# Kernel tuning notes

Measured on AMD Instinct MI355X. Metric: run time of the kernel, lower is better.

Reference implementation:

```python
import jax, jax.numpy as jnp
import numpy as np


def _binarize_ste(w):
    # forward: sign(w) in {-1, +1}; backward: identity (straight-through)
    wb = jnp.where(w >= 0, 1.0, -1.0).astype(w.dtype)
    return w + jax.lax.stop_gradient(wb - w)


def setup_inputs() -> dict:
    key = jax.random.key(0)
    k1, k2 = jax.random.split(key)
    IN, OUT, N = 2048, 2048, 8192
    x = jax.random.normal(k1, (N, IN), dtype=jnp.float32)
    # kaiming_uniform-like init: U(-bound, bound), bound = sqrt(6/in)*? (gain sqrt(5) default in torch)
    bound = float(np.sqrt(6.0 / IN))
    weight = jax.random.uniform(k2, (OUT, IN), dtype=jnp.float32, minval=-bound, maxval=bound)
    bias = jnp.zeros((OUT,), dtype=jnp.float32)
    return {"x": x, "weight": weight, "bias": bias}


def reference(x, weight, bias):
    w_binary = _binarize_ste(weight)  # [out, in], values in {-1, +1}
    # F.linear: x @ W^T + b
    return jnp.einsum('ni,oi->no', x, w_binary) + bias
```

## Files before the change

kernel.cpp:

```cpp
#include <hip/hip_runtime.h>
#include <stdint.h>


typedef __bf16 bf16x8 __attribute__((ext_vector_type(8)));
typedef float f32x4 __attribute__((ext_vector_type(4)));

typedef const __attribute__((address_space(1))) void* gas_ptr;
typedef __attribute__((address_space(3))) void* lds_ptr;

__device__ __forceinline__ unsigned short f2bf_rne(float f) {
    unsigned int u = __builtin_bit_cast(unsigned int, f);
    u += 0x7fffu + ((u >> 16) & 1u);
    return (unsigned short)(u >> 16);
}

__global__ __launch_bounds__(256) void cvt_x_kernel(const float* __restrict__ in,
                                                    unsigned short* __restrict__ out,
                                                    int n8) {
    int i = blockIdx.x * 256 + threadIdx.x;
    if (i >= n8) return;
    const float4* p = reinterpret_cast<const float4*>(in + (size_t)i * 8);
    float4 f0 = p[0], f1 = p[1];
    union { unsigned short s[8]; uint4 v; } o;
    o.s[0] = f2bf_rne(f0.x); o.s[1] = f2bf_rne(f0.y);
    o.s[2] = f2bf_rne(f0.z); o.s[3] = f2bf_rne(f0.w);
    o.s[4] = f2bf_rne(f1.x); o.s[5] = f2bf_rne(f1.y);
    o.s[6] = f2bf_rne(f1.z); o.s[7] = f2bf_rne(f1.w);
    *reinterpret_cast<uint4*>(out + (size_t)i * 8) = o.v;
}

__global__ __launch_bounds__(256) void bin_w_kernel(const float* __restrict__ in,
                                                    unsigned short* __restrict__ out,
                                                    int n4) {
    int i = blockIdx.x * 256 + threadIdx.x;
    if (i >= n4) return;
    float4 f = reinterpret_cast<const float4*>(in)[i];
    union { unsigned short s[4]; uint2 v; } o;
    o.s[0] = (f.x >= 0.f) ? 0x3F80u : 0xBF80u;
    o.s[1] = (f.y >= 0.f) ? 0x3F80u : 0xBF80u;
    o.s[2] = (f.z >= 0.f) ? 0x3F80u : 0xBF80u;
    o.s[3] = (f.w >= 0.f) ? 0x3F80u : 0xBF80u;
    reinterpret_cast<uint2*>(out)[i] = o.v;
}

#define WAITVM(N) asm volatile("s_waitcnt vmcnt(" #N ")" ::: "memory")

__device__ __forceinline__ void block_bar() {
    asm volatile("" ::: "memory");
    __builtin_amdgcn_s_barrier();
    asm volatile("" ::: "memory");
}

__global__ __launch_bounds__(512, 2) void gemm_bin_kernel(
    const unsigned short* __restrict__ A,
    const unsigned short* __restrict__ B,
    const float* __restrict__ bias,
    float* __restrict__ C,
    int M, int N, int K)
{
    __shared__ __align__(16) unsigned char smem_raw[131072];
    unsigned short* const sm = (unsigned short*)smem_raw;

    const int tid  = threadIdx.x;
    const int lane = tid & 63;
    const int wave = tid >> 6;
    const int wm   = wave >> 2;
    const int wn   = wave & 3;
    const int bm   = blockIdx.y;
    const int bn   = blockIdx.x;

    const unsigned short* __restrict__ Agb = A + (size_t)(bm * 256) * K;
    const unsigned short* __restrict__ Bgb = B + (size_t)(bn * 256) * K;

    const int r15 = lane & 15;
    const int kc  = lane >> 4;
    const int sw  = ((r15 >> 2) & 1) << 1;

    const int baseA0 = wm * 8192 + r15 * 64 + ((kc    ) ^ sw) * 8;
    const int baseA1 = wm * 8192 + r15 * 64 + ((kc + 4) ^ sw) * 8;
    const int bBq    = 16384 + (wn >> 1) * 8192 + (wn & 1) * 4096 + r15 * 64;
    const int baseB0 = bBq + ((kc    ) ^ sw) * 8;
    const int baseB1 = bBq + ((kc + 4) ^ sw) * 8;

    int gsoff[2], ldoff[2];
#pragma unroll
    for (int j = 0; j < 2; ++j) {
        const int g  = j * 512 + tid;
        const int rl = g >> 3;
        const int c  = (g & 7) ^ (((rl >> 2) & 1) << 1);
        gsoff[j] = rl * K + c * 8;
        ldoff[j] = g * 8;
    }

    const int colb = bn * 256 + wn * 64;
    float bv[4];
#pragma unroll
    for (int nf = 0; nf < 4; ++nf) {
        bv[nf] = bias[colb + nf * 16 + r15];
        asm volatile("" :: "v"(bv[nf]));
    }

    f32x4 acc[8][4];
#pragma unroll
    for (int m = 0; m < 8; ++m)
#pragma unroll
        for (int n = 0; n < 4; ++n)
#pragma unroll
            for (int r = 0; r < 4; ++r) acc[m][n][r] = 0.f;

    bf16x8 bfr[4][2];

    auto stageAll = [&](int T1, unsigned short* dst) {
        const unsigned short* ga = Agb + (size_t)T1 * 64;
        const unsigned short* gb = Bgb + (size_t)T1 * 64;
#pragma unroll
        for (int j = 0; j < 2; ++j)
            __builtin_amdgcn_global_load_lds((gas_ptr)(ga + gsoff[j]),
                                             (lds_ptr)(dst + ldoff[j]), 16, 0, 0);
#pragma unroll
        for (int j = 0; j < 2; ++j)
            __builtin_amdgcn_global_load_lds((gas_ptr)(ga + (size_t)128 * K + gsoff[j]),
                                             (lds_ptr)(dst + 8192 + ldoff[j]), 16, 0, 0);
#pragma unroll
        for (int j = 0; j < 2; ++j)
            __builtin_amdgcn_global_load_lds((gas_ptr)(gb + gsoff[j]),
                                             (lds_ptr)(dst + 16384 + ldoff[j]), 16, 0, 0);
#pragma unroll
        for (int j = 0; j < 2; ++j)
            __builtin_amdgcn_global_load_lds((gas_ptr)(gb + (size_t)128 * K + gsoff[j]),
                                             (lds_ptr)(dst + 24576 + ldoff[j]), 16, 0, 0);
    };

    const int KT = K >> 6;

    stageAll(0, sm);
    WAITVM(0);
    block_bar();

    for (int T = 0; T < KT; ++T) {
        const unsigned short* bb = sm + (T & 1) * 32768;
        unsigned short* nb = sm + ((T + 1) & 1) * 32768;
#pragma unroll
        for (int mh = 0; mh < 4; ++mh) {
            if (mh == 0) {
                if (T + 1 < KT) stageAll(T + 1, nb);
#pragma unroll
                for (int nf = 0; nf < 4; ++nf) {
                    bfr[nf][0] = *reinterpret_cast<const bf16x8*>(bb + baseB0 + nf * 1024);
                    bfr[nf][1] = *reinterpret_cast<const bf16x8*>(bb + baseB1 + nf * 1024);
                }
            }
            bf16x8 af[2][2];
#pragma unroll
            for (int mi = 0; mi < 2; ++mi) {
                af[mi][0] = *reinterpret_cast<const bf16x8*>(bb + baseA0 + (mh * 2 + mi) * 1024);
                af[mi][1] = *reinterpret_cast<const bf16x8*>(bb + baseA1 + (mh * 2 + mi) * 1024);
            }
            block_bar();
            asm volatile("s_waitcnt lgkmcnt(0)" ::: "memory");
            __builtin_amdgcn_sched_barrier(0);
            __builtin_amdgcn_s_setprio(1);
#pragma unroll
            for (int kk = 0; kk < 2; ++kk)
#pragma unroll
                for (int mi = 0; mi < 2; ++mi)
#pragma unroll
                    for (int nf = 0; nf < 4; ++nf)
                        acc[mh * 2 + mi][nf] = __builtin_amdgcn_mfma_f32_16x16x32_bf16(
                            af[mi][kk], bfr[nf][kk], acc[mh * 2 + mi][nf], 0, 0, 0);
            __builtin_amdgcn_sched_barrier(0);
            __builtin_amdgcn_s_setprio(0);
            if (mh == 3) { WAITVM(0); }
            block_bar();
        }
    }

    const int row0 = bm * 256 + wm * 128 + kc * 4;
#pragma unroll
    for (int mf = 0; mf < 8; ++mf)
#pragma unroll
        for (int nf = 0; nf < 4; ++nf) {
            float* cp = C + (size_t)(row0 + mf * 16) * N + colb + nf * 16 + r15;
#pragma unroll
            for (int r = 0; r < 4; ++r)
                cp[(size_t)r * N] = acc[mf][nf][r] + bv[nf];
        }
}

extern "C" void kernel_launch(void* const* d_in, const int* in_sizes, int n_in,
                              void* d_out, int out_size, void* d_ws, size_t ws_size,
                              hipStream_t stream) {
    const float* x    = (const float*)d_in[0];
    const float* w    = (const float*)d_in[1];
    const float* bias = (const float*)d_in[2];
    float* out = (float*)d_out;

    const int K = 2048;
    const int N = in_sizes[2];
    const int M = in_sizes[0] / K;

    unsigned short* xb = (unsigned short*)d_ws;
    unsigned short* wb = xb + (size_t)M * K;

    const int nx8 = (M * K) / 8;
    const int nw4 = (N * K) / 4;
    cvt_x_kernel<<<(nx8 + 255) / 256, 256, 0, stream>>>(x, xb, nx8);
    bin_w_kernel<<<(nw4 + 255) / 256, 256, 0, stream>>>(w, wb, nw4);

    dim3 grid(N / 256, M / 256);
    gemm_bin_kernel<<<grid, 512, 0, stream>>>(xb, wb, bias, out, M, N, K);
}
```

Measured before the change: 198.9 us.

## Merge prep kernels and split global-to-LDS prefetch across MFMA phases

The two preprocessing kernels (x conversion to bf16 and weight binarization) are merged into one launch that splits its blocks by index, removing one kernel launch. In the GEMM main loop, the next tile's global-to-LDS loads are split so that A is issued in the first sub-phase and B in the second, instead of all at once. The LDS waits are relaxed to lgkmcnt(8) before the barrier, and most compiler sched barriers and memory clobbers are removed so the compiler has more freedom. The aim is to overlap memory issue with MFMA work and cut launch overhead. The cost is that the weaker fencing and partial lgkm waits could allow reordering that hurts the schedule or correctness.

```diff
diff --git a/kernel.cpp b/kernel.cpp
--- a/kernel.cpp
+++ b/kernel.cpp
@@ -14,42 +14,41 @@
     return (unsigned short)(u >> 16);
 }
 
-__global__ __launch_bounds__(256) void cvt_x_kernel(const float* __restrict__ in,
-                                                    unsigned short* __restrict__ out,
-                                                    int n8) {
-    int i = blockIdx.x * 256 + threadIdx.x;
-    if (i >= n8) return;
-    const float4* p = reinterpret_cast<const float4*>(in + (size_t)i * 8);
-    float4 f0 = p[0], f1 = p[1];
-    union { unsigned short s[8]; uint4 v; } o;
-    o.s[0] = f2bf_rne(f0.x); o.s[1] = f2bf_rne(f0.y);
-    o.s[2] = f2bf_rne(f0.z); o.s[3] = f2bf_rne(f0.w);
-    o.s[4] = f2bf_rne(f1.x); o.s[5] = f2bf_rne(f1.y);
-    o.s[6] = f2bf_rne(f1.z); o.s[7] = f2bf_rne(f1.w);
-    *reinterpret_cast<uint4*>(out + (size_t)i * 8) = o.v;
-}
-
-__global__ __launch_bounds__(256) void bin_w_kernel(const float* __restrict__ in,
-                                                    unsigned short* __restrict__ out,
-                                                    int n4) {
-    int i = blockIdx.x * 256 + threadIdx.x;
-    if (i >= n4) return;
-    float4 f = reinterpret_cast<const float4*>(in)[i];
-    union { unsigned short s[4]; uint2 v; } o;
-    o.s[0] = (f.x >= 0.f) ? 0x3F80u : 0xBF80u;
-    o.s[1] = (f.y >= 0.f) ? 0x3F80u : 0xBF80u;
-    o.s[2] = (f.z >= 0.f) ? 0x3F80u : 0xBF80u;
-    o.s[3] = (f.w >= 0.f) ? 0x3F80u : 0xBF80u;
-    reinterpret_cast<uint2*>(out)[i] = o.v;
-}
-
-#define WAITVM(N) asm volatile("s_waitcnt vmcnt(" #N ")" ::: "memory")
-
-__device__ __forceinline__ void block_bar() {
-    asm volatile("" ::: "memory");
-    __builtin_amdgcn_s_barrier();
-    asm volatile("" ::: "memory");
-}
+__global__ __launch_bounds__(256) void prep_kernel(
+    const float* __restrict__ x, const float* __restrict__ w,
+    unsigned short* __restrict__ xb, unsigned short* __restrict__ wb,
+    int nx8, int nxB, int nw4)
+{
+    const int b = blockIdx.x;
+    if (b < nxB) {
+        int i = b * 256 + threadIdx.x;
+        if (i >= nx8) return;
+        const float4* p = reinterpret_cast<const float4*>(x + (size_t)i * 8);
+        float4 f0 = p[0], f1 = p[1];
+        union { unsigned short s[8]; uint4 v; } o;
+        o.s[0] = f2bf_rne(f0.x); o.s[1] = f2bf_rne(f0.y);
+        o.s[2] = f2bf_rne(f0.z); o.s[3] = f2bf_rne(f0.w);
+        o.s[4] = f2bf_rne(f1.x); o.s[5] = f2bf_rne(f1.y);
+        o.s[6] = f2bf_rne(f1.z); o.s[7] = f2bf_rne(f1.w);
+        *reinterpret_cast<uint4*>(xb + (size_t)i * 8) = o.v;
+    } else {
+        int i = (b - nxB) * 256 + threadIdx.x;
+        if (i >= nw4) return;
+        float4 f = reinterpret_cast<const float4*>(w)[i];
+        union { unsigned short s[4]; uint2 v; } o;
+        o.s[0] = (f.x >= 0.f) ? 0x3F80u : 0xBF80u;
+        o.s[1] = (f.y >= 0.f) ? 0x3F80u : 0xBF80u;
+        o.s[2] = (f.z >= 0.f) ? 0x3F80u : 0xBF80u;
+        o.s[3] = (f.w >= 0.f) ? 0x3F80u : 0xBF80u;
+        reinterpret_cast<uint2*>(wb)[i] = o.v;
+    }
+}
+
+#define WAITLGKM0 asm volatile("s_waitcnt lgkmcnt(0)")
+#define WAITLGKM8 asm volatile("s_waitcnt lgkmcnt(8)")
+#define WAITVM0   asm volatile("s_waitcnt vmcnt(0)")
+#define SBAR      __builtin_amdgcn_s_barrier()
+#define SCHEDB    __builtin_amdgcn_sched_barrier(0)
 
 __global__ __launch_bounds__(512, 2) void gemm_bin_kernel(
     const unsigned short* __restrict__ A,
@@ -110,40 +109,34 @@
 
     bf16x8 bfr[4][2];
 
-    auto stageAll = [&](int T1, unsigned short* dst) {
-        const unsigned short* ga = Agb + (size_t)T1 * 64;
-        const unsigned short* gb = Bgb + (size_t)T1 * 64;
+    auto stage2 = [&](const unsigned short* gsrc, unsigned short* dst) {
 #pragma unroll
         for (int j = 0; j < 2; ++j)
-            __builtin_amdgcn_global_load_lds((gas_ptr)(ga + gsoff[j]),
+            __builtin_amdgcn_global_load_lds((gas_ptr)(gsrc + gsoff[j]),
                                              (lds_ptr)(dst + ldoff[j]), 16, 0, 0);
-#pragma unroll
-        for (int j = 0; j < 2; ++j)
-            __builtin_amdgcn_global_load_lds((gas_ptr)(ga + (size_t)128 * K + gsoff[j]),
-                                             (lds_ptr)(dst + 8192 + ldoff[j]), 16, 0, 0);
-#pragma unroll
-        for (int j = 0; j < 2; ++j)
-            __builtin_amdgcn_global_load_lds((gas_ptr)(gb + gsoff[j]),
-                                             (lds_ptr)(dst + 16384 + ldoff[j]), 16, 0, 0);
-#pragma unroll
-        for (int j = 0; j < 2; ++j)
-            __builtin_amdgcn_global_load_lds((gas_ptr)(gb + (size_t)128 * K + gsoff[j]),
-                                             (lds_ptr)(dst + 24576 + ldoff[j]), 16, 0, 0);
     };
 
     const int KT = K >> 6;
 
-    stageAll(0, sm);
-    WAITVM(0);
-    block_bar();
+    stage2(Agb,                   sm);
+    stage2(Agb + (size_t)128 * K, sm + 8192);
+    stage2(Bgb,                   sm + 16384);
+    stage2(Bgb + (size_t)128 * K, sm + 24576);
+    WAITVM0;
+    SBAR;
+    SCHEDB;
+    asm volatile("" ::: "memory");
 
     for (int T = 0; T < KT; ++T) {
         const unsigned short* bb = sm + (T & 1) * 32768;
         unsigned short* nb = sm + ((T + 1) & 1) * 32768;
+        const int pf = (T + 1 < KT);
+        const unsigned short* gaN = Agb + (size_t)(T + 1) * 64;
+        const unsigned short* gbN = Bgb + (size_t)(T + 1) * 64;
+
 #pragma unroll
         for (int mh = 0; mh < 4; ++mh) {
             if (mh == 0) {
-                if (T + 1 < KT) stageAll(T + 1, nb);
 #pragma unroll
                 for (int nf = 0; nf < 4; ++nf) {
                     bfr[nf][0] = *reinterpret_cast<const bf16x8*>(bb + baseB0 + nf * 1024);
@@ -156,9 +149,17 @@
                 af[mi][0] = *reinterpret_cast<const bf16x8*>(bb + baseA0 + (mh * 2 + mi) * 1024);
                 af[mi][1] = *reinterpret_cast<const bf16x8*>(bb + baseA1 + (mh * 2 + mi) * 1024);
             }
-            block_bar();
-            asm volatile("s_waitcnt lgkmcnt(0)" ::: "memory");
-            __builtin_amdgcn_sched_barrier(0);
+            if (mh == 0 && pf) {
+                stage2(gaN,                   nb);
+                stage2(gaN + (size_t)128 * K, nb + 8192);
+            }
+            if (mh == 1 && pf) {
+                stage2(gbN,                   nb + 16384);
+                stage2(gbN + (size_t)128 * K, nb + 24576);
+            }
+            if (mh == 0) WAITLGKM8;
+            SBAR;
+            WAITLGKM0;
             __builtin_amdgcn_s_setprio(1);
 #pragma unroll
             for (int kk = 0; kk < 2; ++kk)
@@ -168,10 +169,13 @@
                     for (int nf = 0; nf < 4; ++nf)
                         acc[mh * 2 + mi][nf] = __builtin_amdgcn_mfma_f32_16x16x32_bf16(
                             af[mi][kk], bfr[nf][kk], acc[mh * 2 + mi][nf], 0, 0, 0);
-            __builtin_amdgcn_sched_barrier(0);
             __builtin_amdgcn_s_setprio(0);
-            if (mh == 3) { WAITVM(0); }
-            block_bar();
+            if (mh == 3) WAITVM0;
+            SBAR;
+            if (mh == 3) {
+                SCHEDB;
+                asm volatile("" ::: "memory");
+            }
         }
     }
 
@@ -204,8 +208,9 @@
 
     const int nx8 = (M * K) / 8;
     const int nw4 = (N * K) / 4;
-    cvt_x_kernel<<<(nx8 + 255) / 256, 256, 0, stream>>>(x, xb, nx8);
-    bin_w_kernel<<<(nw4 + 255) / 256, 256, 0, stream>>>(w, wb, nw4);
+    const int nxB = (nx8 + 255) / 256;
+    const int nwB = (nw4 + 255) / 256;
+    prep_kernel<<<nxB + nwB, 256, 0, stream>>>(x, w, xb, wb, nx8, nxB, nw4);
 
     dim3 grid(N / 256, M / 256);
     gemm_bin_kernel<<<grid, 512, 0, stream>>>(xb, wb, bias, out, M, N, K);
```

After: 191.3 us. -3.8%, faster.
